# Optimization experiments

Hardware: AMD Instinct MI355X
Metric: run time of the kernel (lower is better)

Reference implementation:

```python
import jax, jax.numpy as jnp
import numpy as np

NUM_TOKEN = 16  # number of joint tokens; each locally-connected position has its own weights


def setup_inputs() -> dict:
    key = jax.random.key(0)
    k1, k2, k3 = jax.random.split(key, 3)
    b, n = 64, 256
    input_size, ff_size, output_size = 2048, 8192, 2048
    T = NUM_TOKEN
    cin, cff, cout = input_size // T, ff_size // T, output_size // T
    x = jax.random.normal(k1, (b, n, input_size), dtype=jnp.float32)
    # LocallyConnected2d weights: independent [out_ch, in_ch] matrix per token position t
    w1 = jax.random.normal(k2, (cff, cin, T), dtype=jnp.float32) * 0.05
    w2 = jax.random.normal(k3, (cout, cff, T), dtype=jnp.float32) * 0.05
    return {"x": x, "w1": w1, "w2": w2}


def reference(x, w1, w2):
    # x: [b, n, f]; reshape(b*n, f//T, T) matches torch's reshape(b*n, f//T, T, 1)
    b, n, f = x.shape
    T = NUM_TOKEN
    xr = x.reshape(b * n, f // T, T)  # [B, Cin, T]
    # LocallyConnected2d with k=1: per-position channel mixing (unfold degenerates to identity)
    h = jnp.einsum('bct,oct->bot', xr, w1)          # [B, Cff, T]
    h = jax.nn.gelu(h, approximate=False)           # nn.GELU default is exact erf form
    # dropout is identity in eval / deterministic reference
    y = jnp.einsum('bct,oct->bot', h, w2)           # [B, Cout, T]
    return y.reshape(b, n, -1)                      # feature index = o*T + t, same as torch
```

## Files before the change

### kernel.cpp

```cpp
#include <hip/hip_runtime.h>
#include <hip/hip_bf16.h>
#include <math.h>


typedef __attribute__((ext_vector_type(8))) short bf16x8;
typedef __attribute__((ext_vector_type(4))) float f32x4;

#define MFMA16(a,b,c) __builtin_amdgcn_mfma_f32_16x16x32_bf16((a),(b),(c),0,0,0)

#define N_ROWS   16384
#define XT_PLANE (16384*128)
#define W_TSTR   65536
#define W_JSTR   16384

static __device__ __forceinline__ unsigned short f2bf(float f){
  union{float f; unsigned u;} v; v.f = f;
  return (unsigned short)((v.u + 0x7FFFu + ((v.u>>16)&1u))>>16);
}
static __device__ __forceinline__ unsigned cvtpk(float lo, float hi){
  unsigned r;
  asm("v_cvt_pk_bf16_f32 %0, %1, %2" : "=v"(r) : "v"(lo), "v"(hi));
  return r;
}
static __device__ __forceinline__ float gelu_fast(float x){
  float x2 = x*x;
  float m  = x*(-1.5957691216f - 0.0713548163f*x2);
  float e  = __expf(m);
  return x*__builtin_amdgcn_rcpf(1.0f + e);
}

typedef __attribute__((address_space(1))) const unsigned int gas_u32;
typedef __attribute__((address_space(3))) unsigned int las_u32;
static __device__ __forceinline__ void gload16(const void* g, void* l){
  __builtin_amdgcn_global_load_lds((gas_u32*)g, (las_u32*)l, 16, 0, 0);
}

__global__ __launch_bounds__(256) void k_packw(const float* __restrict__ w1,
                                               const float* __restrict__ w2,
                                               unsigned short* __restrict__ w1p,
                                               unsigned short* __restrict__ w2p){
  int g = blockIdx.x*256 + threadIdx.x;
  bool is1 = (g < 131072);
  int gg = is1 ? g : (g - 131072);
  int l  = gg & 63, q = (l>>4), i = l & 15;
  int ks = (gg>>6)&3, m8 = (gg>>8)&7, jc = (gg>>11)&3, t = (gg>>13)&15;
  union { unsigned short s[8]; bf16x8 v; } u;
  if (is1){
    int o  = jc*128 + m8*16 + i;
    int c0 = ks*32 + q*8;
    #pragma unroll
    for (int j=0;j<8;++j) u.s[j] = f2bf(w1[(o*128 + c0 + j)*16 + t]);
    *(bf16x8*)(w1p + (size_t)gg*8) = u.v;
  } else {
    int o2  = m8*16 + i;
    int cf0 = jc*128 + ks*32 + q*8;
    #pragma unroll
    for (int j=0;j<8;++j) u.s[j] = f2bf(w2[(o2*512 + cf0 + j)*16 + t]);
    *(bf16x8*)(w2p + (size_t)gg*8) = u.v;
  }
}

__global__ __launch_bounds__(256) void k_xt(const float* __restrict__ x,
                                            unsigned short* __restrict__ xt){
  __shared__ unsigned short ls[8*16*136];
  const int r0 = blockIdx.x*8;
  const int tid = threadIdx.x;
  #pragma unroll
  for (int it=0; it<16; ++it){
    int f4  = it*256 + tid;
    int row = f4>>9, rem = f4&511;
    int c = rem>>2, t0 = (rem&3)*4;
    float4 v = *(const float4*)(x + (size_t)(r0+row)*2048 + rem*4);
    ls[(row*16 + t0+0)*136 + c] = f2bf(v.x);
    ls[(row*16 + t0+1)*136 + c] = f2bf(v.y);
    ls[(row*16 + t0+2)*136 + c] = f2bf(v.z);
    ls[(row*16 + t0+3)*136 + c] = f2bf(v.w);
  }
  __syncthreads();
  const int t = tid>>4, cg = tid&15;
  #pragma unroll
  for (int r=0;r<8;++r){
    bf16x8 v = *(const bf16x8*)(ls + (r*16 + t)*136 + cg*8);
    *(bf16x8*)(xt + (size_t)t*XT_PLANE + (size_t)(r0+r)*128 + cg*8) = v;
  }
}

__global__ __launch_bounds__(256,2) void k_ffn(const unsigned short* __restrict__ xt,
                                               const unsigned short* __restrict__ w1p,
                                               const unsigned short* __restrict__ w2p,
                                               unsigned short* __restrict__ yt){
  __shared__ unsigned short ws[2*16384];
  const int bx = blockIdx.x;
  const int t = bx>>7, rt = bx&127, r0 = rt<<7;
  const int tid = threadIdx.x;
  const int wv = tid>>6, l = tid&63, q = l>>4, i = l&15;

  const unsigned short* w1t = w1p + (size_t)t*W_TSTR;
  const unsigned short* w2t = w2p + (size_t)t*W_TSTR;

  auto stage = [&](int hc, int buf){
    const int jc = hc>>1, half = hc&1;
    const unsigned short* w1c = w1t + jc*W_JSTR + half*8192;
    const unsigned short* w2c = w2t + jc*W_JSTR + half*1024;
    unsigned short* Wb = ws + buf*16384;
    #pragma unroll
    for (int c=0;c<8;++c){
      int k = wv*8 + c;
      if (k < 16){
        gload16(w1c + k*512 + l*8, Wb + k*512 + l*8);
      } else {
        int f = k - 16;
        gload16(w2c + (f>>1)*2048 + (f&1)*512 + l*8, Wb + 8192 + f*512 + l*8);
      }
    }
  };

  stage(0, 0);

  bf16x8 xb[4][2];
  {
    const unsigned short* xp = xt + (size_t)t*XT_PLANE + (size_t)(r0 + wv*32)*128;
    #pragma unroll
    for (int ks=0; ks<4; ++ks){
      xb[ks][0] = *(const bf16x8*)(xp + (size_t)i*128 + ks*32 + q*8);
      xb[ks][1] = *(const bf16x8*)(xp + (size_t)(i+16)*128 + ks*32 + q*8);
    }
  }
  __syncthreads();

  f32x4 accY[2][8];
  #pragma unroll
  for (int a=0;a<2;++a)
    #pragma unroll
    for (int b=0;b<8;++b) accY[a][b] = (f32x4){0.f,0.f,0.f,0.f};

  const int idxA = ((q&1)*32 + i)*4;
  const int idxB = idxA + 64;
  const int lo32 = (l < 32);

  int cur = 0;
  #pragma unroll 1
  for (int hc=0; hc<8; ++hc){
    if (hc < 7) stage(hc+1, cur^1);

    const unsigned short* W1 = ws + cur*16384;
    const unsigned short* W2 = W1 + 8192;

    f32x4 acc1[4][2];
    #pragma unroll
    for (int a=0;a<4;++a){ acc1[a][0]=(f32x4){0,0,0,0}; acc1[a][1]=(f32x4){0,0,0,0}; }
    #pragma unroll
    for (int ks=0; ks<4; ++ks){
      #pragma unroll
      for (int mt=0; mt<4; ++mt){
        bf16x8 af = *(const bf16x8*)(W1 + (mt*4+ks)*512 + l*8);
        acc1[mt][0] = MFMA16(af, xb[ks][0], acc1[mt][0]);
        acc1[mt][1] = MFMA16(af, xb[ks][1], acc1[mt][1]);
      }
    }

    unsigned pk[4][2][2];
    #pragma unroll
    for (int mt=0; mt<4; ++mt)
      #pragma unroll
      for (int nt=0; nt<2; ++nt){
        f32x4 v = acc1[mt][nt];
        pk[mt][nt][0] = cvtpk(gelu_fast(v.x), gelu_fast(v.y));
        pk[mt][nt][1] = cvtpk(gelu_fast(v.z), gelu_fast(v.w));
      }

    #pragma unroll
    for (int ks2=0; ks2<2; ++ks2){
      bf16x8 a2[2];
      #pragma unroll
      for (int nt=0; nt<2; ++nt){
        int pA0=(int)pk[2*ks2  ][nt][0], pA1=(int)pk[2*ks2  ][nt][1];
        int pB0=(int)pk[2*ks2+1][nt][0], pB1=(int)pk[2*ks2+1][nt][1];
        int a0 = __builtin_amdgcn_ds_bpermute(idxA, pA0);
        int b0 = __builtin_amdgcn_ds_bpermute(idxA, pB0);
        int a1 = __builtin_amdgcn_ds_bpermute(idxA, pA1);
        int b1 = __builtin_amdgcn_ds_bpermute(idxA, pB1);
        int a2r= __builtin_amdgcn_ds_bpermute(idxB, pA0);
        int b2 = __builtin_amdgcn_ds_bpermute(idxB, pB0);
        int a3 = __builtin_amdgcn_ds_bpermute(idxB, pA1);
        int b3 = __builtin_amdgcn_ds_bpermute(idxB, pB1);
        union{ int ii[4]; bf16x8 v; } u;
        u.ii[0] = lo32 ? a0 : b0;
        u.ii[1] = lo32 ? a1 : b1;
        u.ii[2] = lo32 ? a2r: b2;
        u.ii[3] = lo32 ? a3 : b3;
        a2[nt] = u.v;
      }
      #pragma unroll
      for (int nt2=0; nt2<8; ++nt2){
        bf16x8 bf = *(const bf16x8*)(W2 + (nt2*2+ks2)*512 + l*8);
        accY[0][nt2] = MFMA16(a2[0], bf, accY[0][nt2]);
        accY[1][nt2] = MFMA16(a2[1], bf, accY[1][nt2]);
      }
    }

    __syncthreads();
    cur ^= 1;
  }

  unsigned short* yp = yt + (size_t)t*XT_PLANE + (size_t)(r0 + wv*32)*128;
  #pragma unroll
  for (int mt2=0; mt2<2; ++mt2)
    #pragma unroll
    for (int nt2=0; nt2<8; ++nt2){
      f32x4 v = accY[mt2][nt2];
      unsigned p01 = cvtpk(v.x, v.y);
      unsigned p23 = cvtpk(v.z, v.w);
      int o = nt2*16 + i;
      int rowb = mt2*16 + q*4;
      yp[(rowb+0)*128 + o] = (unsigned short)(p01 & 0xffffu);
      yp[(rowb+1)*128 + o] = (unsigned short)(p01 >> 16);
      yp[(rowb+2)*128 + o] = (unsigned short)(p23 & 0xffffu);
      yp[(rowb+3)*128 + o] = (unsigned short)(p23 >> 16);
    }
}

__global__ __launch_bounds__(256) void k_out(const unsigned short* __restrict__ yt,
                                             float* __restrict__ out){
  __shared__ float ls[4*2176];
  const int r0 = blockIdx.x*4;
  const int tid = threadIdx.x;
  const int t = tid>>4, og = tid&15;
  #pragma unroll
  for (int r=0;r<4;++r){
    bf16x8 v = *(const bf16x8*)(yt + (size_t)t*XT_PLANE + (size_t)(r0+r)*128 + og*8);
    #pragma unroll
    for (int j=0;j<8;++j){
      union{unsigned u; float f;} c; c.u = ((unsigned)(unsigned short)v[j])<<16;
      ls[r*2176 + (og*8+j)*17 + t] = c.f;
    }
  }
  __syncthreads();
  #pragma unroll
  for (int r=0;r<4;++r)
    #pragma unroll
    for (int it=0; it<2; ++it){
      int f4 = it*256 + tid; int o = f4>>2; int t0 = (f4&3)*4;
      const float* p = ls + r*2176 + o*17 + t0;
      float4 v; v.x=p[0]; v.y=p[1]; v.z=p[2]; v.w=p[3];
      *(float4*)(out + (size_t)(r0+r)*2048 + (size_t)f4*4) = v;
    }
}

__global__ __launch_bounds__(128) void k_naive(const float* __restrict__ x,
                                               const float* __restrict__ w1,
                                               const float* __restrict__ w2,
                                               float* __restrict__ out){
  int bid = blockIdx.x; int t = bid & 15; int row = bid >> 4;
  int tid = threadIdx.x;
  __shared__ float xsm[128]; __shared__ float hsm[512];
  xsm[tid] = x[(size_t)row*2048 + tid*16 + t];
  __syncthreads();
  for (int kk=0; kk<4; ++kk){
    int o = kk*128 + tid; float a = 0.f;
    for (int c=0;c<128;++c) a += xsm[c]*w1[(o*128+c)*16+t];
    hsm[o] = 0.5f*a*(1.0f+erff(a*0.70710678f));
  }
  __syncthreads();
  float a = 0.f;
  for (int cf=0; cf<512; ++cf) a += hsm[cf]*w2[(tid*512+cf)*16+t];
  out[(size_t)row*2048 + tid*16 + t] = a;
}

extern "C" void kernel_launch(void* const* d_in, const int* in_sizes, int n_in,
                              void* d_out, int out_size, void* d_ws, size_t ws_size,
                              hipStream_t stream){
  const float* x  = (const float*)d_in[0];
  const float* w1 = (const float*)d_in[1];
  const float* w2 = (const float*)d_in[2];
  float* out = (float*)d_out;

  const size_t NEEDED = 71303168ULL;
  if (ws_size < NEEDED || d_ws == nullptr){
    k_naive<<<dim3(16384*16), dim3(128), 0, stream>>>(x, w1, w2, out);
    return;
  }
  unsigned short* xt  = (unsigned short*)d_ws;
  unsigned short* w1p = xt + 33554432;
  unsigned short* w2p = w1p + 1048576;

  k_packw<<<dim3(1024), dim3(256), 0, stream>>>(w1, w2, w1p, w2p);
  k_xt  <<<dim3(2048), dim3(256), 0, stream>>>(x, xt);
  k_ffn <<<dim3(2048), dim3(256), 0, stream>>>(xt, w1p, w2p, xt);
  k_out <<<dim3(4096), dim3(256), 0, stream>>>(xt, out);
}
```

Measured before the change: 378.4 us.

## Rework input and output transposes with LDS transpose reads and register-only unpack

The input transpose kernel now packs fp32 to bf16 with a packed convert, stores contiguous 8-byte chunks to LDS, and uses ds_read_b64_tr_b16 transposing reads to emit token-planar rows. The output kernel drops its LDS staging and barrier. Each thread loads four token planes and assembles float4 outputs directly in registers, with twice as many rows per block. The goal is to cut the scalar LDS scatter, bank conflicts and sync overhead in the two memory-bound layout kernels. The cost is less coalesced 8-byte global stores in k_xt and a reliance on exact transpose-read semantics.

```diff
diff --git a/kernel.cpp b/kernel.cpp
--- a/kernel.cpp
+++ b/kernel.cpp
@@ -21,6 +21,12 @@
   unsigned r;
   asm("v_cvt_pk_bf16_f32 %0, %1, %2" : "=v"(r) : "v"(lo), "v"(hi));
   return r;
+}
+static __device__ __forceinline__ float bflo(unsigned u){
+  union{unsigned x; float f;} c; c.x = u<<16; return c.f;
+}
+static __device__ __forceinline__ float bfhi(unsigned u){
+  union{unsigned x; float f;} c; c.x = u & 0xffff0000u; return c.f;
 }
 static __device__ __forceinline__ float gelu_fast(float x){
   float x2 = x*x;
@@ -33,6 +39,9 @@
 typedef __attribute__((address_space(3))) unsigned int las_u32;
 static __device__ __forceinline__ void gload16(const void* g, void* l){
   __builtin_amdgcn_global_load_lds((gas_u32*)g, (las_u32*)l, 16, 0, 0);
+}
+static __device__ __forceinline__ unsigned lds_off(const void* p){
+  return (unsigned)(size_t)(const __attribute__((address_space(3))) void*)p;
 }
 
 __global__ __launch_bounds__(256) void k_packw(const float* __restrict__ w1,
@@ -60,28 +69,51 @@
   }
 }
 
+#define TRRD(d, a, OFS) asm volatile("ds_read_b64_tr_b16 %0, %1 offset:" OFS \
+                                     : "=v"(d) : "v"(a))
 __global__ __launch_bounds__(256) void k_xt(const float* __restrict__ x,
                                             unsigned short* __restrict__ xt){
-  __shared__ unsigned short ls[8*16*136];
+  __shared__ unsigned short ls[8*2048];
   const int r0 = blockIdx.x*8;
   const int tid = threadIdx.x;
   #pragma unroll
   for (int it=0; it<16; ++it){
-    int f4  = it*256 + tid;
-    int row = f4>>9, rem = f4&511;
-    int c = rem>>2, t0 = (rem&3)*4;
+    int idx = it*256 + tid;
+    int row = idx>>9, rem = idx&511;
     float4 v = *(const float4*)(x + (size_t)(r0+row)*2048 + rem*4);
-    ls[(row*16 + t0+0)*136 + c] = f2bf(v.x);
-    ls[(row*16 + t0+1)*136 + c] = f2bf(v.y);
-    ls[(row*16 + t0+2)*136 + c] = f2bf(v.z);
-    ls[(row*16 + t0+3)*136 + c] = f2bf(v.w);
+    unsigned lo = cvtpk(v.x, v.y), hi = cvtpk(v.z, v.w);
+    unsigned long long p = ((unsigned long long)hi<<32) | lo;
+    *(unsigned long long*)(ls + row*2048 + rem*4) = p;
   }
   __syncthreads();
-  const int t = tid>>4, cg = tid&15;
-  #pragma unroll
-  for (int r=0;r<8;++r){
-    bf16x8 v = *(const bf16x8*)(ls + (r*16 + t)*136 + cg*8);
-    *(bf16x8*)(xt + (size_t)t*XT_PLANE + (size_t)(r0+r)*128 + cg*8) = v;
+  const int wv = tid>>6, l = tid&63, g = l>>4, i = l&15;
+  unsigned base = lds_off(ls) + (unsigned)wv*8192u + (unsigned)l*8u;
+  #pragma unroll
+  for (int rr=0; rr<2; ++rr){
+    unsigned long long d0,d1,d2,d3,d4,d5,d6,d7;
+    if (rr==0){
+      TRRD(d0, base, "0");    TRRD(d1, base, "512");
+      TRRD(d2, base, "1024"); TRRD(d3, base, "1536");
+      TRRD(d4, base, "2048"); TRRD(d5, base, "2560");
+      TRRD(d6, base, "3072"); TRRD(d7, base, "3584");
+    } else {
+      TRRD(d0, base, "4096"); TRRD(d1, base, "4608");
+      TRRD(d2, base, "5120"); TRRD(d3, base, "5632");
+      TRRD(d4, base, "6144"); TRRD(d5, base, "6656");
+      TRRD(d6, base, "7168"); TRRD(d7, base, "7680");
+    }
+    asm volatile("s_waitcnt lgkmcnt(0)" ::: "memory");
+    __builtin_amdgcn_sched_barrier(0);
+    unsigned short* xp = xt + (size_t)i*XT_PLANE
+                       + (size_t)(r0 + 2*wv + rr)*128 + g*4;
+    *(unsigned long long*)(xp + 0*16)  = d0;
+    *(unsigned long long*)(xp + 1*16)  = d1;
+    *(unsigned long long*)(xp + 2*16)  = d2;
+    *(unsigned long long*)(xp + 3*16)  = d3;
+    *(unsigned long long*)(xp + 4*16)  = d4;
+    *(unsigned long long*)(xp + 5*16)  = d5;
+    *(unsigned long long*)(xp + 6*16)  = d6;
+    *(unsigned long long*)(xp + 7*16)  = d7;
   }
 }
 
@@ -222,29 +254,30 @@
 
 __global__ __launch_bounds__(256) void k_out(const unsigned short* __restrict__ yt,
                                              float* __restrict__ out){
-  __shared__ float ls[4*2176];
-  const int r0 = blockIdx.x*4;
+  const int r0 = blockIdx.x*8;
   const int tid = threadIdx.x;
-  const int t = tid>>4, og = tid&15;
-  #pragma unroll
-  for (int r=0;r<4;++r){
-    bf16x8 v = *(const bf16x8*)(yt + (size_t)t*XT_PLANE + (size_t)(r0+r)*128 + og*8);
-    #pragma unroll
-    for (int j=0;j<8;++j){
-      union{unsigned u; float f;} c; c.u = ((unsigned)(unsigned short)v[j])<<16;
-      ls[r*2176 + (og*8+j)*17 + t] = c.f;
-    }
-  }
-  __syncthreads();
-  #pragma unroll
-  for (int r=0;r<4;++r)
-    #pragma unroll
-    for (int it=0; it<2; ++it){
-      int f4 = it*256 + tid; int o = f4>>2; int t0 = (f4&3)*4;
-      const float* p = ls + r*2176 + o*17 + t0;
-      float4 v; v.x=p[0]; v.y=p[1]; v.z=p[2]; v.w=p[3];
-      *(float4*)(out + (size_t)(r0+r)*2048 + (size_t)f4*4) = v;
-    }
+  const int r = tid>>5, w = tid&31;
+  const int og = w&15, tq0 = w>>4;
+  #pragma unroll
+  for (int it=0; it<2; ++it){
+    int tq = tq0 + it*2;
+    const unsigned short* yp = yt + (size_t)(tq*4)*XT_PLANE
+                             + (size_t)(r0+r)*128 + og*8;
+    union{ bf16x8 v; unsigned u[4]; } y0, y1, y2, y3;
+    y0.v = *(const bf16x8*)(yp);
+    y1.v = *(const bf16x8*)(yp + XT_PLANE);
+    y2.v = *(const bf16x8*)(yp + 2*XT_PLANE);
+    y3.v = *(const bf16x8*)(yp + 3*XT_PLANE);
+    float* op = out + (size_t)(r0+r)*2048 + og*128 + tq*4;
+    #pragma unroll
+    for (int k=0;k<8;++k){
+      unsigned w0 = y0.u[k>>1], w1 = y1.u[k>>1], w2 = y2.u[k>>1], w3 = y3.u[k>>1];
+      f32x4 o4;
+      if (k&1){ o4.x=bfhi(w0); o4.y=bfhi(w1); o4.z=bfhi(w2); o4.w=bfhi(w3); }
+      else    { o4.x=bflo(w0); o4.y=bflo(w1); o4.z=bflo(w2); o4.w=bflo(w3); }
+      *(f32x4*)(op + k*16) = o4;
+    }
+  }
 }
 
 __global__ __launch_bounds__(128) void k_naive(const float* __restrict__ x,
@@ -287,5 +320,5 @@
   k_packw<<<dim3(1024), dim3(256), 0, stream>>>(w1, w2, w1p, w2p);
   k_xt  <<<dim3(2048), dim3(256), 0, stream>>>(x, xt);
   k_ffn <<<dim3(2048), dim3(256), 0, stream>>>(xt, w1p, w2p, xt);
-  k_out <<<dim3(4096), dim3(256), 0, stream>>>(xt, out);
-}
+  k_out <<<dim3(2048), dim3(256), 0, stream>>>(xt, out);
+}
```

Result: slower. 404.1 us (+6.8%).
